# Kernel tuning notes

Hardware: AMD Instinct MI355X
Metric: run time of the kernel (lower is better)

Reference implementation:

```python
import jax, jax.numpy as jnp
import numpy as np


def _euler_xyz_to_matrix(angles):
    """pytorch3d euler_angles_to_matrix with convention 'XYZ'.
    angles: [..., 3] -> R = Rx(a0) @ Ry(a1) @ Rz(a2), shape [..., 3, 3]."""
    ax, ay, az = angles[..., 0], angles[..., 1], angles[..., 2]
    cx, sx = jnp.cos(ax), jnp.sin(ax)
    cy, sy = jnp.cos(ay), jnp.sin(ay)
    cz, sz = jnp.cos(az), jnp.sin(az)
    one = jnp.ones_like(cx)
    zero = jnp.zeros_like(cx)
    Rx = jnp.stack([one, zero, zero,
                    zero, cx, -sx,
                    zero, sx, cx], axis=-1).reshape(angles.shape[:-1] + (3, 3))
    Ry = jnp.stack([cy, zero, sy,
                    zero, one, zero,
                    -sy, zero, cy], axis=-1).reshape(angles.shape[:-1] + (3, 3))
    Rz = jnp.stack([cz, -sz, zero,
                    sz, cz, zero,
                    zero, zero, one], axis=-1).reshape(angles.shape[:-1] + (3, 3))
    return Rx @ Ry @ Rz


def setup_inputs() -> dict:
    key = jax.random.key(0)
    k1, k2, k3, k4, k5 = jax.random.split(key, 5)
    B, S, P, V = 16, 16, 64, 2562
    scales = jax.random.uniform(k1, (B, S, 1), dtype=jnp.float32) + 0.5
    transforms = jax.random.normal(k2, (B, S, P, 6), dtype=jnp.float32)
    prototype_weights = jax.random.uniform(k3, (B, S, P), dtype=jnp.float32)
    prototype_offsets = 0.1 * jax.random.normal(k4, (P, V, 3), dtype=jnp.float32)
    bv = jax.random.normal(k5, (V, 3), dtype=jnp.float32)
    base_verts = bv / jnp.linalg.norm(bv, axis=-1, keepdims=True)  # unit sphere
    return {"scales": scales, "transforms": transforms,
            "prototype_weights": prototype_weights,
            "prototype_offsets": prototype_offsets,
            "base_verts": base_verts}


def reference(scales, transforms, prototype_weights, prototype_offsets, base_verts):
    B, S, P = prototype_weights.shape
    V = base_verts.shape[0]
    translation = transforms[..., :3]          # [B,S,P,3]
    rotation = transforms[..., 3:]             # [B,S,P,3]
    R = _euler_xyz_to_matrix(rotation)         # [B,S,P,3,3]
    deformed = base_verts[None] + prototype_offsets  # [P,V,3]
    # per-(b,s,p): out += w * (scale * (deformed @ R^T) + t)
    # fold weight*scale into R, reduce over p in one contraction
    ws = prototype_weights * scales            # [B,S,P]
    Rws = R * ws[..., None, None]              # [B,S,P,3,3]
    rotated = jnp.einsum('bspij,pvj->bsvi', Rws, deformed)  # [B,S,V,3]
    trans = jnp.einsum('bsp,bspi->bsi', prototype_weights, translation)  # [B,S,3]
    out = rotated + trans[:, :, None, :]       # [B,S,V,3]
    return out.reshape(B * S, V, 3)
```

## Files before the change

### kernel.cpp

```cpp
#include <hip/hip_runtime.h>

#define NP 64
#define NV 2562
#define KK 192
#define NROWS_B 2592
#define GXN 81
#define GYM 8

typedef short bf16x8 __attribute__((ext_vector_type(8)));
typedef float f32x4  __attribute__((ext_vector_type(4)));

static __device__ __forceinline__ unsigned short f2bf(float x) {
    unsigned u = __float_as_uint(x);
    return (unsigned short)((u + 0x7fffu + ((u >> 16) & 1u)) >> 16);
}

__global__ __launch_bounds__(256) void prep_kernel(
    const float* __restrict__ scales,
    const float* __restrict__ transforms,
    const float* __restrict__ weights,
    const float* __restrict__ offsets,
    unsigned short* __restrict__ A,
    unsigned short* __restrict__ Bt,
    float* __restrict__ aux)
{
    const int blk = blockIdx.x;
    const int t   = threadIdx.x;

    if (blk < 64) {
        const int wave = t >> 6;
        const int p    = t & 63;
        const int bs   = blk * 4 + wave;

        const float* tr = transforms + ((size_t)bs * NP + p) * 6;
        const float tx = tr[0], ty = tr[1], tz = tr[2];
        const float ax = tr[3], ay = tr[4], az = tr[5];
        const float wgt = weights[bs * NP + p];
        const float ws  = wgt * scales[bs];

        float sx, cx, sy, cy, sz, cz;
        __sincosf(ax, &sx, &cx);
        __sincosf(ay, &sy, &cy);
        __sincosf(az, &sz, &cz);

        float v12[12];
        v12[0] = (cy * cz) * ws;
        v12[1] = (-cy * sz) * ws;
        v12[2] = (sy) * ws;
        v12[3] = (cx * sz + sx * sy * cz) * ws;
        v12[4] = (cx * cz - sx * sy * sz) * ws;
        v12[5] = (-sx * cy) * ws;
        v12[6] = (sx * sz - cx * sy * cz) * ws;
        v12[7] = (sx * cz + cx * sy * sz) * ws;
        v12[8] = (cx * cy) * ws;
        v12[9]  = wgt * tx;
        v12[10] = wgt * ty;
        v12[11] = wgt * tz;

#pragma unroll
        for (int i = 0; i < 3; ++i) {
            unsigned short* row = A + ((size_t)(bs * 4 + i)) * KK + p * 3;
            row[0] = f2bf(v12[i * 3 + 0]);
            row[1] = f2bf(v12[i * 3 + 1]);
            row[2] = f2bf(v12[i * 3 + 2]);
        }
        {
            unsigned short* row = A + ((size_t)(bs * 4 + 3)) * KK + p * 3;
            row[0] = 0; row[1] = 0; row[2] = 0;
        }

        float red[12];
#pragma unroll
        for (int k = 0; k < 12; ++k) red[k] = v12[k];
#pragma unroll
        for (int m = 1; m < 64; m <<= 1) {
#pragma unroll
            for (int k = 0; k < 12; ++k) red[k] += __shfl_xor(red[k], m);
        }
        if (p == 0) {
#pragma unroll
            for (int k = 0; k < 12; ++k) aux[bs * 12 + k] = red[k];
        }
    } else {
        const int vloc = t >> 3;
        const int pc   = t & 7;
        const int v    = (blk - 64) * 32 + vloc;
        const bool live = (v < NV);

        unsigned short tmp[24];
#pragma unroll
        for (int pi = 0; pi < 8; ++pi) {
            const int p = pc * 8 + pi;
            float o0 = 0.f, o1 = 0.f, o2 = 0.f;
            if (live) {
                const float* o = offsets + ((size_t)p * NV + v) * 3;
                o0 = o[0]; o1 = o[1]; o2 = o[2];
            }
            tmp[pi * 3 + 0] = f2bf(o0);
            tmp[pi * 3 + 1] = f2bf(o1);
            tmp[pi * 3 + 2] = f2bf(o2);
        }
        uint4* dst = (uint4*)(Bt + (size_t)v * KK + pc * 24);
        dst[0] = *(const uint4*)(tmp);
        dst[1] = *(const uint4*)(tmp + 8);
        dst[2] = *(const uint4*)(tmp + 16);
    }
}

__global__ __launch_bounds__(256) void gemm_kernel(
    const unsigned short* __restrict__ A,
    const unsigned short* __restrict__ Bt,
    const float* __restrict__ aux,
    const float* __restrict__ bverts,
    float* __restrict__ out)
{
    const int t    = threadIdx.x;
    const int w    = t >> 6;
    const int lane = t & 63;
    const int q    = lane >> 4;
    const int r16  = lane & 15;

    const int np0 = blockIdx.x * 32;
    const int mt0 = blockIdx.y * 8 + w * 2;

    const unsigned short* ap0 = A  + ((size_t)(mt0 * 16) + r16) * KK + q * 8;
    const unsigned short* ap1 = ap0 + 16 * KK;
    const unsigned short* bp0 = Bt + ((size_t)np0 + r16) * KK + q * 8;
    const unsigned short* bp1 = bp0 + 16 * KK;

    f32x4 acc00 = {0,0,0,0}, acc01 = {0,0,0,0};
    f32x4 acc10 = {0,0,0,0}, acc11 = {0,0,0,0};

#pragma unroll
    for (int ks = 0; ks < 6; ++ks) {
        bf16x8 a0 = *(const bf16x8*)(ap0 + ks * 32);
        bf16x8 a1 = *(const bf16x8*)(ap1 + ks * 32);
        bf16x8 b0 = *(const bf16x8*)(bp0 + ks * 32);
        bf16x8 b1 = *(const bf16x8*)(bp1 + ks * 32);
        acc00 = __builtin_amdgcn_mfma_f32_16x16x32_bf16(a0, b0, acc00, 0, 0, 0);
        acc01 = __builtin_amdgcn_mfma_f32_16x16x32_bf16(a0, b1, acc01, 0, 0, 0);
        acc10 = __builtin_amdgcn_mfma_f32_16x16x32_bf16(a1, b0, acc10, 0, 0, 0);
        acc11 = __builtin_amdgcn_mfma_f32_16x16x32_bf16(a1, b1, acc11, 0, 0, 0);
    }

    const int v0 = np0 + r16;
    const int v1 = v0 + 16;
    float b0x = 0, b0y = 0, b0z = 0, b1x = 0, b1y = 0, b1z = 0;
    if (v0 < NV) { const float* b = bverts + (size_t)v0 * 3; b0x = b[0]; b0y = b[1]; b0z = b[2]; }
    if (v1 < NV) { const float* b = bverts + (size_t)v1 * 3; b1x = b[0]; b1y = b[1]; b1z = b[2]; }

#pragma unroll
    for (int mi = 0; mi < 2; ++mi) {
        const int bs = (mt0 + mi) * 4 + q;
        const float4 R0 = *(const float4*)(aux + bs * 12);
        const float4 R1 = *(const float4*)(aux + bs * 12 + 4);
        const float4 R2 = *(const float4*)(aux + bs * 12 + 8);
        const f32x4 a0 = mi ? acc10 : acc00;
        const f32x4 a1 = mi ? acc11 : acc01;

        if (v0 < NV) {
            float* po = out + ((size_t)bs * NV + v0) * 3;
            po[0] = a0[0] + R0.x * b0x + R0.y * b0y + R0.z * b0z + R2.y;
            po[1] = a0[1] + R0.w * b0x + R1.x * b0y + R1.y * b0z + R2.z;
            po[2] = a0[2] + R1.z * b0x + R1.w * b0y + R2.x * b0z + R2.w;
        }
        if (v1 < NV) {
            float* po = out + ((size_t)bs * NV + v1) * 3;
            po[0] = a1[0] + R0.x * b1x + R0.y * b1y + R0.z * b1z + R2.y;
            po[1] = a1[1] + R0.w * b1x + R1.x * b1y + R1.y * b1z + R2.z;
            po[2] = a1[2] + R1.z * b1x + R1.w * b1y + R2.x * b1z + R2.w;
        }
    }
}

extern "C" void kernel_launch(void* const* d_in, const int* in_sizes, int n_in,
                              void* d_out, int out_size, void* d_ws, size_t ws_size,
                              hipStream_t stream) {
    const float* scales     = (const float*)d_in[0];
    const float* transforms = (const float*)d_in[1];
    const float* weights    = (const float*)d_in[2];
    const float* offsets    = (const float*)d_in[3];
    const float* bverts     = (const float*)d_in[4];
    float* out = (float*)d_out;

    unsigned short* A  = (unsigned short*)d_ws;
    unsigned short* Bt = A + (size_t)1024 * KK;
    float* aux = (float*)(Bt + (size_t)NROWS_B * KK);

    prep_kernel<<<dim3(64 + GXN), dim3(256), 0, stream>>>(
        scales, transforms, weights, offsets, A, Bt, aux);

    gemm_kernel<<<dim3(GXN, GYM), dim3(256), 0, stream>>>(A, Bt, aux, bverts, out);
}
```

Baseline: 78.32 us.

## Fuse prep and GEMM into one kernel staging operands in LDS

Merges the preprocessing kernel and the MFMA GEMM kernel into a single launch. Each block recomputes its own A tile (rotation matrices for 32 batch rows) and B tile (bf16 offsets for 32 vertices) directly into padded shared memory, then runs the MFMA loop from LDS. This removes a kernel launch and the global-memory round trip through the workspace. In exchange the sin/cos work is redone in each of the 81 column blocks and the offsets are reloaded by each of the 8 row blocks.

```diff
diff --git a/kernel.cpp b/kernel.cpp
--- a/kernel.cpp
+++ b/kernel.cpp
@@ -3,91 +3,44 @@
 #define NP 64
 #define NV 2562
 #define KK 192
-#define NROWS_B 2592
+#define LDP 200
 #define GXN 81
 #define GYM 8
 
 typedef short bf16x8 __attribute__((ext_vector_type(8)));
 typedef float f32x4  __attribute__((ext_vector_type(4)));
+typedef unsigned int u32x4 __attribute__((ext_vector_type(4)));
 
 static __device__ __forceinline__ unsigned short f2bf(float x) {
     unsigned u = __float_as_uint(x);
     return (unsigned short)((u + 0x7fffu + ((u >> 16) & 1u)) >> 16);
 }
-
-__global__ __launch_bounds__(256) void prep_kernel(
+static __device__ __forceinline__ unsigned pack2(float lo, float hi) {
+    return (unsigned)f2bf(lo) | ((unsigned)f2bf(hi) << 16);
+}
+
+__global__ __launch_bounds__(256) void fused_kernel(
     const float* __restrict__ scales,
     const float* __restrict__ transforms,
     const float* __restrict__ weights,
     const float* __restrict__ offsets,
-    unsigned short* __restrict__ A,
-    unsigned short* __restrict__ Bt,
-    float* __restrict__ aux)
+    const float* __restrict__ bverts,
+    float* __restrict__ out)
 {
-    const int blk = blockIdx.x;
-    const int t   = threadIdx.x;
-
-    if (blk < 64) {
-        const int wave = t >> 6;
-        const int p    = t & 63;
-        const int bs   = blk * 4 + wave;
-
-        const float* tr = transforms + ((size_t)bs * NP + p) * 6;
-        const float tx = tr[0], ty = tr[1], tz = tr[2];
-        const float ax = tr[3], ay = tr[4], az = tr[5];
-        const float wgt = weights[bs * NP + p];
-        const float ws  = wgt * scales[bs];
-
-        float sx, cx, sy, cy, sz, cz;
-        __sincosf(ax, &sx, &cx);
-        __sincosf(ay, &sy, &cy);
-        __sincosf(az, &sz, &cz);
-
-        float v12[12];
-        v12[0] = (cy * cz) * ws;
-        v12[1] = (-cy * sz) * ws;
-        v12[2] = (sy) * ws;
-        v12[3] = (cx * sz + sx * sy * cz) * ws;
-        v12[4] = (cx * cz - sx * sy * sz) * ws;
-        v12[5] = (-sx * cy) * ws;
-        v12[6] = (sx * sz - cx * sy * cz) * ws;
-        v12[7] = (sx * cz + cx * sy * sz) * ws;
-        v12[8] = (cx * cy) * ws;
-        v12[9]  = wgt * tx;
-        v12[10] = wgt * ty;
-        v12[11] = wgt * tz;
-
-#pragma unroll
-        for (int i = 0; i < 3; ++i) {
-            unsigned short* row = A + ((size_t)(bs * 4 + i)) * KK + p * 3;
-            row[0] = f2bf(v12[i * 3 + 0]);
-            row[1] = f2bf(v12[i * 3 + 1]);
-            row[2] = f2bf(v12[i * 3 + 2]);
-        }
-        {
-            unsigned short* row = A + ((size_t)(bs * 4 + 3)) * KK + p * 3;
-            row[0] = 0; row[1] = 0; row[2] = 0;
-        }
-
-        float red[12];
-#pragma unroll
-        for (int k = 0; k < 12; ++k) red[k] = v12[k];
-#pragma unroll
-        for (int m = 1; m < 64; m <<= 1) {
-#pragma unroll
-            for (int k = 0; k < 12; ++k) red[k] += __shfl_xor(red[k], m);
-        }
-        if (p == 0) {
-#pragma unroll
-            for (int k = 0; k < 12; ++k) aux[bs * 12 + k] = red[k];
-        }
-    } else {
+    __shared__ __align__(16) unsigned short Ash[128 * LDP];
+    __shared__ __align__(16) unsigned short Bsh[32 * LDP];
+    __shared__ __align__(16) float auxsh[32 * 12];
+
+    const int t  = threadIdx.x;
+    const int bx = blockIdx.x;
+    const int by = blockIdx.y;
+
+    {
         const int vloc = t >> 3;
         const int pc   = t & 7;
-        const int v    = (blk - 64) * 32 + vloc;
+        const int v    = bx * 32 + vloc;
         const bool live = (v < NV);
-
-        unsigned short tmp[24];
+        float f[24];
 #pragma unroll
         for (int pi = 0; pi < 8; ++pi) {
             const int p = pc * 8 + pi;
@@ -96,54 +49,128 @@
                 const float* o = offsets + ((size_t)p * NV + v) * 3;
                 o0 = o[0]; o1 = o[1]; o2 = o[2];
             }
-            tmp[pi * 3 + 0] = f2bf(o0);
-            tmp[pi * 3 + 1] = f2bf(o1);
-            tmp[pi * 3 + 2] = f2bf(o2);
-        }
-        uint4* dst = (uint4*)(Bt + (size_t)v * KK + pc * 24);
-        dst[0] = *(const uint4*)(tmp);
-        dst[1] = *(const uint4*)(tmp + 8);
-        dst[2] = *(const uint4*)(tmp + 16);
-    }
-}
-
-__global__ __launch_bounds__(256) void gemm_kernel(
-    const unsigned short* __restrict__ A,
-    const unsigned short* __restrict__ Bt,
-    const float* __restrict__ aux,
-    const float* __restrict__ bverts,
-    float* __restrict__ out)
-{
-    const int t    = threadIdx.x;
+            f[pi * 3 + 0] = o0; f[pi * 3 + 1] = o1; f[pi * 3 + 2] = o2;
+        }
+        unsigned short* d = Bsh + vloc * LDP + pc * 24;
+        u32x4 w0 = { pack2(f[0],f[1]),   pack2(f[2],f[3]),   pack2(f[4],f[5]),   pack2(f[6],f[7]) };
+        u32x4 w1 = { pack2(f[8],f[9]),   pack2(f[10],f[11]), pack2(f[12],f[13]), pack2(f[14],f[15]) };
+        u32x4 w2 = { pack2(f[16],f[17]), pack2(f[18],f[19]), pack2(f[20],f[21]), pack2(f[22],f[23]) };
+        *reinterpret_cast<u32x4*>(d)      = w0;
+        *reinterpret_cast<u32x4*>(d + 8)  = w1;
+        *reinterpret_cast<u32x4*>(d + 16) = w2;
+    }
+
+    {
+        const int bsl = t >> 3;
+        const int pg  = t & 7;
+        const int bs  = by * 32 + bsl;
+        const float sc = scales[bs];
+
+        float racc[12];
+#pragma unroll
+        for (int k = 0; k < 12; ++k) racc[k] = 0.f;
+        unsigned aw[36];
+#pragma unroll
+        for (int k = 0; k < 36; ++k) aw[k] = 0u;
+
+#pragma unroll
+        for (int pi = 0; pi < 8; ++pi) {
+            const int p = pg * 8 + pi;
+            const float* tr = transforms + ((size_t)bs * NP + p) * 6;
+            const float tx = tr[0], ty = tr[1], tz = tr[2];
+            const float ax = tr[3], ay = tr[4], az = tr[5];
+            const float wgt = weights[bs * NP + p];
+            const float ws  = wgt * sc;
+
+            float sx, cx, sy, cy, sz, cz;
+            __sincosf(ax, &sx, &cx);
+            __sincosf(ay, &sy, &cy);
+            __sincosf(az, &sz, &cz);
+
+            float r[12];
+            r[0] = (cy * cz) * ws;
+            r[1] = (-cy * sz) * ws;
+            r[2] = (sy) * ws;
+            r[3] = (cx * sz + sx * sy * cz) * ws;
+            r[4] = (cx * cz - sx * sy * sz) * ws;
+            r[5] = (-sx * cy) * ws;
+            r[6] = (sx * sz - cx * sy * cz) * ws;
+            r[7] = (sx * cz + cx * sy * sz) * ws;
+            r[8] = (cx * cy) * ws;
+            r[9]  = wgt * tx;
+            r[10] = wgt * ty;
+            r[11] = wgt * tz;
+
+#pragma unroll
+            for (int k = 0; k < 12; ++k) racc[k] += r[k];
+#pragma unroll
+            for (int i = 0; i < 3; ++i) {
+#pragma unroll
+                for (int j = 0; j < 3; ++j) {
+                    const int s = pi * 3 + j;
+                    aw[i * 12 + (s >> 1)] |= ((unsigned)f2bf(r[i * 3 + j])) << (16 * (s & 1));
+                }
+            }
+        }
+
+        unsigned short* arow = Ash + (bsl * 4) * LDP + pg * 24;
+#pragma unroll
+        for (int i = 0; i < 3; ++i) {
+            unsigned short* d = arow + i * LDP;
+            u32x4 w0 = { aw[i*12+0], aw[i*12+1], aw[i*12+2],  aw[i*12+3]  };
+            u32x4 w1 = { aw[i*12+4], aw[i*12+5], aw[i*12+6],  aw[i*12+7]  };
+            u32x4 w2 = { aw[i*12+8], aw[i*12+9], aw[i*12+10], aw[i*12+11] };
+            *reinterpret_cast<u32x4*>(d)      = w0;
+            *reinterpret_cast<u32x4*>(d + 8)  = w1;
+            *reinterpret_cast<u32x4*>(d + 16) = w2;
+        }
+        {
+            unsigned short* d = arow + 3 * LDP;
+            u32x4 z = {0u, 0u, 0u, 0u};
+            *reinterpret_cast<u32x4*>(d)      = z;
+            *reinterpret_cast<u32x4*>(d + 8)  = z;
+            *reinterpret_cast<u32x4*>(d + 16) = z;
+        }
+
+#pragma unroll
+        for (int m = 1; m < 8; m <<= 1) {
+#pragma unroll
+            for (int k = 0; k < 12; ++k) racc[k] += __shfl_xor(racc[k], m);
+        }
+        if (pg == 0) {
+#pragma unroll
+            for (int k = 0; k < 12; ++k) auxsh[bsl * 12 + k] = racc[k];
+        }
+    }
+
+    __syncthreads();
+
     const int w    = t >> 6;
     const int lane = t & 63;
     const int q    = lane >> 4;
     const int r16  = lane & 15;
 
-    const int np0 = blockIdx.x * 32;
-    const int mt0 = blockIdx.y * 8 + w * 2;
-
-    const unsigned short* ap0 = A  + ((size_t)(mt0 * 16) + r16) * KK + q * 8;
-    const unsigned short* ap1 = ap0 + 16 * KK;
-    const unsigned short* bp0 = Bt + ((size_t)np0 + r16) * KK + q * 8;
-    const unsigned short* bp1 = bp0 + 16 * KK;
+    const unsigned short* ap0 = Ash + (w * 32 + r16) * LDP + q * 8;
+    const unsigned short* ap1 = ap0 + 16 * LDP;
+    const unsigned short* bp0 = Bsh + r16 * LDP + q * 8;
+    const unsigned short* bp1 = bp0 + 16 * LDP;
 
     f32x4 acc00 = {0,0,0,0}, acc01 = {0,0,0,0};
     f32x4 acc10 = {0,0,0,0}, acc11 = {0,0,0,0};
 
 #pragma unroll
     for (int ks = 0; ks < 6; ++ks) {
-        bf16x8 a0 = *(const bf16x8*)(ap0 + ks * 32);
-        bf16x8 a1 = *(const bf16x8*)(ap1 + ks * 32);
-        bf16x8 b0 = *(const bf16x8*)(bp0 + ks * 32);
-        bf16x8 b1 = *(const bf16x8*)(bp1 + ks * 32);
+        bf16x8 a0 = *reinterpret_cast<const bf16x8*>(ap0 + ks * 32);
+        bf16x8 a1 = *reinterpret_cast<const bf16x8*>(ap1 + ks * 32);
+        bf16x8 b0 = *reinterpret_cast<const bf16x8*>(bp0 + ks * 32);
+        bf16x8 b1 = *reinterpret_cast<const bf16x8*>(bp1 + ks * 32);
         acc00 = __builtin_amdgcn_mfma_f32_16x16x32_bf16(a0, b0, acc00, 0, 0, 0);
         acc01 = __builtin_amdgcn_mfma_f32_16x16x32_bf16(a0, b1, acc01, 0, 0, 0);
         acc10 = __builtin_amdgcn_mfma_f32_16x16x32_bf16(a1, b0, acc10, 0, 0, 0);
         acc11 = __builtin_amdgcn_mfma_f32_16x16x32_bf16(a1, b1, acc11, 0, 0, 0);
     }
 
-    const int v0 = np0 + r16;
+    const int v0 = bx * 32 + r16;
     const int v1 = v0 + 16;
     float b0x = 0, b0y = 0, b0z = 0, b1x = 0, b1y = 0, b1z = 0;
     if (v0 < NV) { const float* b = bverts + (size_t)v0 * 3; b0x = b[0]; b0y = b[1]; b0z = b[2]; }
@@ -151,10 +178,11 @@
 
 #pragma unroll
     for (int mi = 0; mi < 2; ++mi) {
-        const int bs = (mt0 + mi) * 4 + q;
-        const float4 R0 = *(const float4*)(aux + bs * 12);
-        const float4 R1 = *(const float4*)(aux + bs * 12 + 4);
-        const float4 R2 = *(const float4*)(aux + bs * 12 + 8);
+        const int bsl = (2 * w + mi) * 4 + q;
+        const int bs  = by * 32 + bsl;
+        const float4 R0 = *reinterpret_cast<const float4*>(auxsh + bsl * 12);
+        const float4 R1 = *reinterpret_cast<const float4*>(auxsh + bsl * 12 + 4);
+        const float4 R2 = *reinterpret_cast<const float4*>(auxsh + bsl * 12 + 8);
         const f32x4 a0 = mi ? acc10 : acc00;
         const f32x4 a1 = mi ? acc11 : acc01;
 
@@ -183,12 +211,8 @@
     const float* bverts     = (const float*)d_in[4];
     float* out = (float*)d_out;
 
-    unsigned short* A  = (unsigned short*)d_ws;
-    unsigned short* Bt = A + (size_t)1024 * KK;
-    float* aux = (float*)(Bt + (size_t)NROWS_B * KK);
-
-    prep_kernel<<<dim3(64 + GXN), dim3(256), 0, stream>>>(
-        scales, transforms, weights, offsets, A, Bt, aux);
-
-    gemm_kernel<<<dim3(GXN, GYM), dim3(256), 0, stream>>>(A, Bt, aux, bverts, out);
-}
+    (void)d_ws; (void)ws_size;
+
+    fused_kernel<<<dim3(GXN, GYM), dim3(256), 0, stream>>>(
+        scales, transforms, weights, offsets, bverts, out);
+}
```

Result: no change. 79.61 us (+1.6%).
